# Performance work log

Measured on AMD Instinct MI355X. Metric: run time of the kernel, lower is better.

Reference implementation:

```python
import jax, jax.numpy as jnp
import numpy as np
import math

INPUT_SIZE = 64  # feature dim D, matches init_kwargs input_size


def setup_inputs() -> dict:
    key = jax.random.key(0)
    k1, k2 = jax.random.split(key)
    B, N, D = 32, 2048, INPUT_SIZE
    x = jax.random.normal(k1, (B, N, D), dtype=jnp.float32)
    adj = jax.random.randint(k2, (N, N), 0, 2, dtype=jnp.int32)
    return {"input": x, "adj": adj}


def reference(input, adj):
    # input: [B, N, D], adj: [N, N]
    scale = 1.0 / math.sqrt(INPUT_SIZE)
    # batched QK^T: [B, N, N]
    scores = jnp.einsum('bnd,bmd->bnm', input, input) * scale
    neg = jnp.float32(-1e12)
    masked = jnp.where(adj > 0, scores, neg)  # adj broadcasts over batch
    attn = jax.nn.softmax(masked, axis=-1)
    # AV: [B, N, D]
    out = jnp.einsum('bnm,bmd->bnd', attn, input)
    return out
```

## Files before the change

kernel.cpp:

```cpp
#include <hip/hip_runtime.h>
#include <hip/hip_bf16.h>

#define NB 32
#define NN 2048
#define DD 64
#define NCH 32
#define LOG2E 1.44269504088896340736f
#define SQC 0.4246613965f

typedef __attribute__((ext_vector_type(8))) short short8;
typedef __attribute__((ext_vector_type(4))) short short4v;
typedef __attribute__((ext_vector_type(4))) float f32x4;

#define MFMA32K(A, B, C) \
  __builtin_amdgcn_mfma_f32_16x16x32_bf16((A), (B), (C), 0, 0, 0)
#define MFMA16(A, B, C) \
  __builtin_amdgcn_mfma_f32_16x16x16bf16_1k((A), (B), (C), 0, 0, 0)

#define GLOAD_LDS16(gp, lp)                                                   \
  __builtin_amdgcn_global_load_lds(                                          \
      (const __attribute__((address_space(1))) void*)(gp),                   \
      (__attribute__((address_space(3))) void*)(lp), 16, 0, 0)

__device__ __forceinline__ short f2bf(float x) {
  __bf16 h = (__bf16)x;
  return __builtin_bit_cast(short, h);
}

__device__ __forceinline__ float fast_exp2(float x) {
#if __has_builtin(__builtin_amdgcn_exp2f)
  return __builtin_amdgcn_exp2f(x);
#else
  return exp2f(x);
#endif
}

__device__ __forceinline__ unsigned pack_bf16_rnd(float lo, float hi) {
  unsigned ulo = __builtin_bit_cast(unsigned, lo) + 0x8000u;
  unsigned uhi = __builtin_bit_cast(unsigned, hi) + 0x8000u;
  return __builtin_amdgcn_perm(uhi, ulo, 0x07060302u);
}

__global__ __launch_bounds__(256) void prep_img(const float* __restrict__ x,
                                                short* __restrict__ img) {
  __shared__ float t[64 * 68];
  const int tid = threadIdx.x;
  const int c = blockIdx.x;
  const int b = blockIdx.y;
  const int r = tid >> 2;
  const int cg = tid & 3;

  const float* src = x + ((size_t)b * NN + c * 64 + r) * DD + cg * 16;
#pragma unroll
  for (int h = 0; h < 4; ++h)
    *(float4*)&t[r * 68 + cg * 16 + h * 4] = ((const float4*)src)[h];
  __syncthreads();

  short* imgc = img + (size_t)(b * NCH + c) * 16 * 512;

#pragma unroll
  for (int i = 0; i < 2; ++i) {
    const int kc = tid + i * 256;
    const int u = kc >> 6, l = kc & 63;
    const int nt = u >> 1, ks = u & 1;
    const float* tr = &t[(nt * 16 + (l & 15)) * 68 + ks * 32 + (l >> 4) * 8];
    short8 v;
#pragma unroll
    for (int j = 0; j < 8; ++j) v[j] = f2bf(tr[j] * SQC);
    *(short8*)&imgc[(size_t)u * 512 + l * 8] = v;
  }
#pragma unroll
  for (int i = 0; i < 2; ++i) {
    const int vc = tid + i * 256;
    const int u = vc >> 6, l = vc & 63;
    const int dt = u >> 1, ntp = u & 1;
    const int d = dt * 16 + (l & 15);
    const int k0 = ntp * 32 + ((l >> 4) << 2);
    short8 o;
#pragma unroll
    for (int h = 0; h < 2; ++h)
#pragma unroll
      for (int r2 = 0; r2 < 4; ++r2)
        o[h * 4 + r2] = f2bf(t[(k0 + h * 16 + r2) * 68 + d]);
    *(short8*)&imgc[(size_t)(8 + u) * 512 + l * 8] = o;
  }
}

__global__ __launch_bounds__(256) void prep_adj(const int* __restrict__ adj,
                                                unsigned long long* __restrict__ bits) {
  const int i = blockIdx.x * 256 + threadIdx.x;
  unsigned long long m = __ballot(adj[i] > 0);
  if ((threadIdx.x & 63) == 0) bits[i >> 6] = m;
}

__device__ __forceinline__ void chunk_body(
    const short* __restrict__ sB, unsigned long long a0, unsigned long long a1,
    int quad, int l, const short8 (&qf)[2][2], const short4v& ones,
    f32x4 (&acc)[2][4], f32x4 (&acc_l)[2]) {
  a0 >>= (quad * 4);
  a1 >>= (quad * 4);
  const unsigned lo0 = (unsigned)a0, hi0 = (unsigned)(a0 >> 32);
  const unsigned lo1 = (unsigned)a1, hi1 = (unsigned)(a1 >> 32);
  const short* sK = sB;
  const short* sV = sB + 4096;

#pragma unroll
  for (int ntp = 0; ntp < 2; ++ntp) {
    short4v pf[2][2];
#pragma unroll
    for (int h = 0; h < 2; ++h) {
      const int nt = ntp * 2 + h;
      f32x4 s0 = {0.f, 0.f, 0.f, 0.f};
      f32x4 s1 = {0.f, 0.f, 0.f, 0.f};
#pragma unroll
      for (int ks = 0; ks < 2; ++ks) {
        short8 kf = *(const short8*)&sK[(nt * 2 + ks) * 512 + l * 8];
        s0 = MFMA32K(kf, qf[0][ks], s0);
        s1 = MFMA32K(kf, qf[1][ks], s1);
      }
      const unsigned w0 = (nt < 2) ? lo0 : hi0;
      const unsigned w1 = (nt < 2) ? lo1 : hi1;
      const int sh = (nt & 1) * 16;
      float p0[4], p1[4];
#pragma unroll
      for (int r = 0; r < 4; ++r) {
        float e0 = fast_exp2(s0[r]);
        float e1 = fast_exp2(s1[r]);
        p0[r] = ((w0 >> (sh + r)) & 1u) ? e0 : 0.f;
        p1[r] = ((w1 >> (sh + r)) & 1u) ? e1 : 0.f;
      }
      uint2 u0, u1;
      u0.x = pack_bf16_rnd(p0[0], p0[1]);
      u0.y = pack_bf16_rnd(p0[2], p0[3]);
      u1.x = pack_bf16_rnd(p1[0], p1[1]);
      u1.y = pack_bf16_rnd(p1[2], p1[3]);
      pf[h][0] = __builtin_bit_cast(short4v, u0);
      pf[h][1] = __builtin_bit_cast(short4v, u1);
      acc_l[0] = MFMA16(ones, pf[h][0], acc_l[0]);
      acc_l[1] = MFMA16(ones, pf[h][1], acc_l[1]);
    }
#pragma unroll
    for (int dt = 0; dt < 4; ++dt) {
      short8 vv = *(const short8*)&sV[(dt * 2 + ntp) * 512 + l * 8];
      short4v vlo, vhi;
      vlo[0] = vv[0]; vlo[1] = vv[1]; vlo[2] = vv[2]; vlo[3] = vv[3];
      vhi[0] = vv[4]; vhi[1] = vv[5]; vhi[2] = vv[6]; vhi[3] = vv[7];
      acc[0][dt] = MFMA16(vlo, pf[0][0], acc[0][dt]);
      acc[1][dt] = MFMA16(vlo, pf[0][1], acc[1][dt]);
      acc[0][dt] = MFMA16(vhi, pf[1][0], acc[0][dt]);
      acc[1][dt] = MFMA16(vhi, pf[1][1], acc[1][dt]);
    }
  }
}

__global__ __launch_bounds__(256, 2) void gat_flash8(
    const short* __restrict__ img, const unsigned long long* __restrict__ adjb,
    float* __restrict__ out) {
  __shared__ short sI[4][8192];

  const int beta = blockIdx.x;
  const int b = (beta & 7) * 4 + (beta >> 7);
  const int xq = (beta >> 3) & 15;

  const int tid = threadIdx.x;
  const int w = tid >> 6;
  const int l = tid & 63;
  const int lane16 = l & 15;
  const int quad = l >> 4;
  const int qbase = xq * 128 + w * 32;

  const short* img_b = img + (size_t)b * NCH * 16 * 512;

  const int qc = xq * 2 + (w >> 1);
  const int ntq0 = (w & 1) * 2;
  short8 qf[2][2];
#pragma unroll
  for (int qt = 0; qt < 2; ++qt)
#pragma unroll
    for (int ks = 0; ks < 2; ++ks)
      qf[qt][ks] = *(const short8*)&img_b[((size_t)qc * 16 +
                                          (ntq0 + qt) * 2 + ks) * 512 + l * 8];

  f32x4 accA[2][4], accB[2][4], aclA[2], aclB[2];
#pragma unroll
  for (int qt = 0; qt < 2; ++qt) {
    aclA[qt] = {0.f, 0.f, 0.f, 0.f};
    aclB[qt] = {0.f, 0.f, 0.f, 0.f};
#pragma unroll
    for (int dt = 0; dt < 4; ++dt) {
      accA[qt][dt] = {0.f, 0.f, 0.f, 0.f};
      accB[qt][dt] = {0.f, 0.f, 0.f, 0.f};
    }
  }
  short4v ones;
  ones[0] = 0x3F80; ones[1] = 0x3F80; ones[2] = 0x3F80; ones[3] = 0x3F80;

  const unsigned long long* ar0 = adjb + (size_t)(qbase + lane16) * NCH;
  const unsigned long long* ar1 = adjb + (size_t)(qbase + 16 + lane16) * NCH;

#pragma unroll
  for (int i = 0; i < 4; ++i) {
    const int u = i * 4 + w;
    GLOAD_LDS16(img_b + (size_t)u * 512 + l * 8, &sI[0][u * 512]);
    GLOAD_LDS16(img_b + (size_t)16 * 8192 + u * 512 + l * 8, &sI[2][u * 512]);
  }
  __syncthreads();

  for (int c = 0; c < 16; ++c) {
    const int cur = c & 1;
    if (c < 15) {
      const short* pA = img_b + (size_t)(c + 1) * 8192;
      const short* pB = img_b + (size_t)(c + 17) * 8192;
#pragma unroll
      for (int i = 0; i < 4; ++i) {
        const int u = i * 4 + w;
        GLOAD_LDS16(pA + (size_t)u * 512 + l * 8, &sI[cur ^ 1][u * 512]);
        GLOAD_LDS16(pB + (size_t)u * 512 + l * 8, &sI[2 + (cur ^ 1)][u * 512]);
      }
    }

    const unsigned long long a0A = ar0[c], a1A = ar1[c];
    const unsigned long long a0B = ar0[c + 16], a1B = ar1[c + 16];

    chunk_body(sI[cur], a0A, a1A, quad, l, qf, ones, accA, aclA);
    chunk_body(sI[2 + cur], a0B, a1B, quad, l, qf, ones, accB, aclB);

    __syncthreads();
  }

#pragma unroll
  for (int qt = 0; qt < 2; ++qt) {
    const float inv = 1.0f / (aclA[qt][0] + aclB[qt][0]);
    float* op =
        out + ((size_t)b * NN + qbase + qt * 16 + lane16) * DD + quad * 4;
#pragma unroll
    for (int dt = 0; dt < 4; ++dt) {
      float4 o;
      o.x = (accA[qt][dt][0] + accB[qt][dt][0]) * inv;
      o.y = (accA[qt][dt][1] + accB[qt][dt][1]) * inv;
      o.z = (accA[qt][dt][2] + accB[qt][dt][2]) * inv;
      o.w = (accA[qt][dt][3] + accB[qt][dt][3]) * inv;
      *(float4*)(op + dt * 16) = o;
    }
  }
}

extern "C" void kernel_launch(void* const* d_in, const int* in_sizes, int n_in,
                              void* d_out, int out_size, void* d_ws,
                              size_t ws_size, hipStream_t stream) {
  const float* x = (const float*)d_in[0];
  const int* adj = (const int*)d_in[1];
  float* out = (float*)d_out;

  short* img = (short*)d_ws;
  unsigned long long* adjb =
      (unsigned long long*)(img + (size_t)NB * NCH * 16 * 512);

  prep_img<<<dim3(NCH, NB), 256, 0, stream>>>(x, img);
  prep_adj<<<(NN * NN) / 256, 256, 0, stream>>>(adj, adjb);
  gat_flash8<<<512, 256, 0, stream>>>(img, adjb, out);
}
```

Measured before the change: 144.6 us.

## Split attention kernel into smaller blocks with staggered chunk order and software-pipelined QK

Replaces the 256-thread, 4-wave kernel that processed two key halves per iteration with a 128-thread, 2-wave kernel launched as 1024 blocks. Each block walks all 32 key chunks starting at a per-block rotated offset. The aim is to spread L2/HBM traffic and cut the shared memory per block. Inside a chunk, the QK MFMAs for the next 16-key tile are issued before the exp/mask/PV work of the current tile, to overlap matrix and vector work. The trade-off is a single accumulator chain per block and more blocks that each reload K/V.

Result: slower. 152.2 us (+5.2%).

```diff
diff --git a/kernel.cpp b/kernel.cpp
--- a/kernel.cpp
+++ b/kernel.cpp
@@ -93,39 +93,116 @@
   if ((threadIdx.x & 63) == 0) bits[i >> 6] = m;
 }
 
-__device__ __forceinline__ void chunk_body(
-    const short* __restrict__ sB, unsigned long long a0, unsigned long long a1,
-    int quad, int l, const short8 (&qf)[2][2], const short4v& ones,
-    f32x4 (&acc)[2][4], f32x4 (&acc_l)[2]) {
-  a0 >>= (quad * 4);
-  a1 >>= (quad * 4);
-  const unsigned lo0 = (unsigned)a0, hi0 = (unsigned)(a0 >> 32);
-  const unsigned lo1 = (unsigned)a1, hi1 = (unsigned)(a1 >> 32);
-  const short* sK = sB;
-  const short* sV = sB + 4096;
-
-#pragma unroll
-  for (int ntp = 0; ntp < 2; ++ntp) {
-    short4v pf[2][2];
-#pragma unroll
-    for (int h = 0; h < 2; ++h) {
-      const int nt = ntp * 2 + h;
-      f32x4 s0 = {0.f, 0.f, 0.f, 0.f};
-      f32x4 s1 = {0.f, 0.f, 0.f, 0.f};
-#pragma unroll
-      for (int ks = 0; ks < 2; ++ks) {
-        short8 kf = *(const short8*)&sK[(nt * 2 + ks) * 512 + l * 8];
-        s0 = MFMA32K(kf, qf[0][ks], s0);
-        s1 = MFMA32K(kf, qf[1][ks], s1);
-      }
-      const unsigned w0 = (nt < 2) ? lo0 : hi0;
-      const unsigned w1 = (nt < 2) ? lo1 : hi1;
-      const int sh = (nt & 1) * 16;
+__global__ __launch_bounds__(128, 2) void gat_flash9(
+    const short* __restrict__ img, const unsigned long long* __restrict__ adjb,
+    float* __restrict__ out) {
+  __shared__ short sI[2][8192];
+
+  const int beta = blockIdx.x;
+  const int xcd = beta & 7;
+  const int idx = beta >> 3;
+  const int bb = idx >> 5;
+  const int xq = idx & 31;
+  const int b = xcd * 4 + bb;
+
+  const int tid = threadIdx.x;
+  const int w = tid >> 6;
+  const int l = tid & 63;
+  const int lane16 = l & 15;
+  const int quad = l >> 4;
+  const int qbase = xq * 64 + w * 32;
+  const int coff = idx & 31;
+
+  const short* img_b = img + (size_t)b * NCH * 8192;
+
+  short8 qf[2][2];
+#pragma unroll
+  for (int qt = 0; qt < 2; ++qt)
+#pragma unroll
+    for (int ks = 0; ks < 2; ++ks)
+      qf[qt][ks] = *(const short8*)&img_b[((size_t)xq * 16 +
+                                          (w * 2 + qt) * 2 + ks) * 512 + l * 8];
+
+  f32x4 acc[2][4];
+  f32x4 acl[2];
+#pragma unroll
+  for (int qt = 0; qt < 2; ++qt) {
+    acl[qt] = {0.f, 0.f, 0.f, 0.f};
+#pragma unroll
+    for (int dt = 0; dt < 4; ++dt) acc[qt][dt] = {0.f, 0.f, 0.f, 0.f};
+  }
+  short4v ones;
+  ones[0] = 0x3F80; ones[1] = 0x3F80; ones[2] = 0x3F80; ones[3] = 0x3F80;
+  const f32x4 zero = {0.f, 0.f, 0.f, 0.f};
+
+  const unsigned long long* ar0 = adjb + (size_t)(qbase + lane16) * NCH;
+  const unsigned long long* ar1 = adjb + (size_t)(qbase + 16 + lane16) * NCH;
+
+  {
+    const short* p = img_b + (size_t)coff * 8192;
+#pragma unroll
+    for (int i = 0; i < 8; ++i) {
+      const int u = i * 2 + w;
+      GLOAD_LDS16(p + (size_t)u * 512 + l * 8, &sI[0][u * 512]);
+    }
+  }
+  __syncthreads();
+
+  for (int ci = 0; ci < NCH; ++ci) {
+    const int c = (ci + coff) & 31;
+    const int cur = ci & 1;
+    if (ci < NCH - 1) {
+      const int cn = (ci + 1 + coff) & 31;
+      const short* p = img_b + (size_t)cn * 8192;
+#pragma unroll
+      for (int i = 0; i < 8; ++i) {
+        const int u = i * 2 + w;
+        GLOAD_LDS16(p + (size_t)u * 512 + l * 8, &sI[cur ^ 1][u * 512]);
+      }
+    }
+
+    const unsigned long long a0 = ar0[c] >> (quad * 4);
+    const unsigned long long a1 = ar1[c] >> (quad * 4);
+    const unsigned m0[2] = {(unsigned)a0, (unsigned)(a0 >> 32)};
+    const unsigned m1[2] = {(unsigned)a1, (unsigned)(a1 >> 32)};
+
+    const short* sKc = sI[cur];
+    const short* sVc = sI[cur] + 4096;
+
+    f32x4 sS[2][2];
+    {
+      short8 k0 = *(const short8*)&sKc[0 * 512 + l * 8];
+      short8 k1 = *(const short8*)&sKc[1 * 512 + l * 8];
+      sS[0][0] = MFMA32K(k0, qf[0][0], zero);
+      sS[0][0] = MFMA32K(k1, qf[0][1], sS[0][0]);
+      sS[0][1] = MFMA32K(k0, qf[1][0], zero);
+      sS[0][1] = MFMA32K(k1, qf[1][1], sS[0][1]);
+    }
+
+    short8 vv[4];
+#pragma unroll
+    for (int nt = 0; nt < 4; ++nt) {
+      const int pp = nt & 1;
+      if (nt < 3) {
+        short8 k0 = *(const short8*)&sKc[((nt + 1) * 2) * 512 + l * 8];
+        short8 k1 = *(const short8*)&sKc[((nt + 1) * 2 + 1) * 512 + l * 8];
+        sS[pp ^ 1][0] = MFMA32K(k0, qf[0][0], zero);
+        sS[pp ^ 1][0] = MFMA32K(k1, qf[0][1], sS[pp ^ 1][0]);
+        sS[pp ^ 1][1] = MFMA32K(k0, qf[1][0], zero);
+        sS[pp ^ 1][1] = MFMA32K(k1, qf[1][1], sS[pp ^ 1][1]);
+      }
+      if (pp == 0) {
+#pragma unroll
+        for (int dt = 0; dt < 4; ++dt)
+          vv[dt] = *(const short8*)&sVc[(dt * 2 + (nt >> 1)) * 512 + l * 8];
+      }
+      const unsigned w0 = m0[nt >> 1], w1 = m1[nt >> 1];
+      const int sh = pp * 16;
       float p0[4], p1[4];
 #pragma unroll
       for (int r = 0; r < 4; ++r) {
-        float e0 = fast_exp2(s0[r]);
-        float e1 = fast_exp2(s1[r]);
+        float e0 = fast_exp2(sS[pp][0][r]);
+        float e1 = fast_exp2(sS[pp][1][r]);
         p0[r] = ((w0 >> (sh + r)) & 1u) ? e0 : 0.f;
         p1[r] = ((w1 >> (sh + r)) & 1u) ? e1 : 0.f;
       }
@@ -134,112 +211,34 @@
       u0.y = pack_bf16_rnd(p0[2], p0[3]);
       u1.x = pack_bf16_rnd(p1[0], p1[1]);
       u1.y = pack_bf16_rnd(p1[2], p1[3]);
-      pf[h][0] = __builtin_bit_cast(short4v, u0);
-      pf[h][1] = __builtin_bit_cast(short4v, u1);
-      acc_l[0] = MFMA16(ones, pf[h][0], acc_l[0]);
-      acc_l[1] = MFMA16(ones, pf[h][1], acc_l[1]);
-    }
-#pragma unroll
-    for (int dt = 0; dt < 4; ++dt) {
-      short8 vv = *(const short8*)&sV[(dt * 2 + ntp) * 512 + l * 8];
-      short4v vlo, vhi;
-      vlo[0] = vv[0]; vlo[1] = vv[1]; vlo[2] = vv[2]; vlo[3] = vv[3];
-      vhi[0] = vv[4]; vhi[1] = vv[5]; vhi[2] = vv[6]; vhi[3] = vv[7];
-      acc[0][dt] = MFMA16(vlo, pf[0][0], acc[0][dt]);
-      acc[1][dt] = MFMA16(vlo, pf[0][1], acc[1][dt]);
-      acc[0][dt] = MFMA16(vhi, pf[1][0], acc[0][dt]);
-      acc[1][dt] = MFMA16(vhi, pf[1][1], acc[1][dt]);
-    }
-  }
-}
-
-__global__ __launch_bounds__(256, 2) void gat_flash8(
-    const short* __restrict__ img, const unsigned long long* __restrict__ adjb,
-    float* __restrict__ out) {
-  __shared__ short sI[4][8192];
-
-  const int beta = blockIdx.x;
-  const int b = (beta & 7) * 4 + (beta >> 7);
-  const int xq = (beta >> 3) & 15;
-
-  const int tid = threadIdx.x;
-  const int w = tid >> 6;
-  const int l = tid & 63;
-  const int lane16 = l & 15;
-  const int quad = l >> 4;
-  const int qbase = xq * 128 + w * 32;
-
-  const short* img_b = img + (size_t)b * NCH * 16 * 512;
-
-  const int qc = xq * 2 + (w >> 1);
-  const int ntq0 = (w & 1) * 2;
-  short8 qf[2][2];
-#pragma unroll
-  for (int qt = 0; qt < 2; ++qt)
-#pragma unroll
-    for (int ks = 0; ks < 2; ++ks)
-      qf[qt][ks] = *(const short8*)&img_b[((size_t)qc * 16 +
-                                          (ntq0 + qt) * 2 + ks) * 512 + l * 8];
-
-  f32x4 accA[2][4], accB[2][4], aclA[2], aclB[2];
+      short4v pf0 = __builtin_bit_cast(short4v, u0);
+      short4v pf1 = __builtin_bit_cast(short4v, u1);
+      acl[0] = MFMA16(ones, pf0, acl[0]);
+      acl[1] = MFMA16(ones, pf1, acl[1]);
+#pragma unroll
+      for (int dt = 0; dt < 4; ++dt) {
+        short4v vh = (pp == 0)
+                         ? __builtin_shufflevector(vv[dt], vv[dt], 0, 1, 2, 3)
+                         : __builtin_shufflevector(vv[dt], vv[dt], 4, 5, 6, 7);
+        acc[0][dt] = MFMA16(vh, pf0, acc[0][dt]);
+        acc[1][dt] = MFMA16(vh, pf1, acc[1][dt]);
+      }
+    }
+    __syncthreads();
+  }
+
 #pragma unroll
   for (int qt = 0; qt < 2; ++qt) {
-    aclA[qt] = {0.f, 0.f, 0.f, 0.f};
-    aclB[qt] = {0.f, 0.f, 0.f, 0.f};
-#pragma unroll
-    for (int dt = 0; dt < 4; ++dt) {
-      accA[qt][dt] = {0.f, 0.f, 0.f, 0.f};
-      accB[qt][dt] = {0.f, 0.f, 0.f, 0.f};
-    }
-  }
-  short4v ones;
-  ones[0] = 0x3F80; ones[1] = 0x3F80; ones[2] = 0x3F80; ones[3] = 0x3F80;
-
-  const unsigned long long* ar0 = adjb + (size_t)(qbase + lane16) * NCH;
-  const unsigned long long* ar1 = adjb + (size_t)(qbase + 16 + lane16) * NCH;
-
-#pragma unroll
-  for (int i = 0; i < 4; ++i) {
-    const int u = i * 4 + w;
-    GLOAD_LDS16(img_b + (size_t)u * 512 + l * 8, &sI[0][u * 512]);
-    GLOAD_LDS16(img_b + (size_t)16 * 8192 + u * 512 + l * 8, &sI[2][u * 512]);
-  }
-  __syncthreads();
-
-  for (int c = 0; c < 16; ++c) {
-    const int cur = c & 1;
-    if (c < 15) {
-      const short* pA = img_b + (size_t)(c + 1) * 8192;
-      const short* pB = img_b + (size_t)(c + 17) * 8192;
-#pragma unroll
-      for (int i = 0; i < 4; ++i) {
-        const int u = i * 4 + w;
-        GLOAD_LDS16(pA + (size_t)u * 512 + l * 8, &sI[cur ^ 1][u * 512]);
-        GLOAD_LDS16(pB + (size_t)u * 512 + l * 8, &sI[2 + (cur ^ 1)][u * 512]);
-      }
-    }
-
-    const unsigned long long a0A = ar0[c], a1A = ar1[c];
-    const unsigned long long a0B = ar0[c + 16], a1B = ar1[c + 16];
-
-    chunk_body(sI[cur], a0A, a1A, quad, l, qf, ones, accA, aclA);
-    chunk_body(sI[2 + cur], a0B, a1B, quad, l, qf, ones, accB, aclB);
-
-    __syncthreads();
-  }
-
-#pragma unroll
-  for (int qt = 0; qt < 2; ++qt) {
-    const float inv = 1.0f / (aclA[qt][0] + aclB[qt][0]);
+    const float inv = 1.0f / acl[qt][0];
     float* op =
         out + ((size_t)b * NN + qbase + qt * 16 + lane16) * DD + quad * 4;
 #pragma unroll
     for (int dt = 0; dt < 4; ++dt) {
       float4 o;
-      o.x = (accA[qt][dt][0] + accB[qt][dt][0]) * inv;
-      o.y = (accA[qt][dt][1] + accB[qt][dt][1]) * inv;
-      o.z = (accA[qt][dt][2] + accB[qt][dt][2]) * inv;
-      o.w = (accA[qt][dt][3] + accB[qt][dt][3]) * inv;
+      o.x = acc[qt][dt][0] * inv;
+      o.y = acc[qt][dt][1] * inv;
+      o.z = acc[qt][dt][2] * inv;
+      o.w = acc[qt][dt][3] * inv;
       *(float4*)(op + dt * 16) = o;
     }
   }
@@ -258,5 +257,5 @@
 
   prep_img<<<dim3(NCH, NB), 256, 0, stream>>>(x, img);
   prep_adj<<<(NN * NN) / 256, 256, 0, stream>>>(adj, adjb);
-  gat_flash8<<<512, 256, 0, stream>>>(img, adjb, out);
-}
+  gat_flash9<<<1024, 128, 0, stream>>>(img, adjb, out);
+}
```
